# Performance work log

Measured on AMD Instinct MI355X. Metric: run time of the kernel, lower is better.

## Reference

```python
import jax, jax.numpy as jnp
import numpy as np

N, D, H, E = 50000, 512, 8, 3200000
DK = D // H  # 64


def setup_inputs() -> dict:
    key = jax.random.key(0)
    ks = jax.random.split(key, 12)
    x = jax.random.normal(ks[0], (N, D), dtype=jnp.float32)
    row_index = jnp.sort(jax.random.randint(ks[1], (E,), 0, N))
    col_index = jax.random.randint(ks[2], (E,), 0, N)
    att_bias = jax.random.normal(ks[3], (H, E), dtype=jnp.float32)
    # xavier-uniform-ish linear params (bias zero per module init)
    lim = np.sqrt(6.0 / (D + D)).astype(np.float32)
    def w(k):
        return jax.random.uniform(k, (D, D), minval=-lim, maxval=lim, dtype=jnp.float32)
    return {
        "x": x, "row_index": row_index, "col_index": col_index, "att_bias": att_bias,
        "Wq": w(ks[4]), "bq": jnp.zeros((D,), jnp.float32),
        "Wk": w(ks[5]), "bk": jnp.zeros((D,), jnp.float32),
        "Wv": w(ks[6]), "bv": jnp.zeros((D,), jnp.float32),
        "Wo": w(ks[7]), "bo": jnp.zeros((D,), jnp.float32),
    }


def _proj(x, W, b):
    # nn.Linear then reshape(N, H, DK).permute(1,0,2) -> [H, N, DK]
    return (x @ W.T + b).reshape(x.shape[0], H, DK).transpose(1, 0, 2)


def reference(x, row_index, col_index, att_bias, Wq, bq, Wk, bk, Wv, bv, Wo, bo):
    q = _proj(x, Wq, bq) / jnp.sqrt(jnp.float32(DK))  # [H,N,DK]
    k = _proj(x, Wk, bk)
    v = _proj(x, Wv, bv)
    n = x.shape[0]
    # masked QK^T at sparse (row,col) entries + additive sparse bias -> [H,E]
    logits = jnp.einsum("hed,hed->he", q[:, row_index], k[:, col_index]) + att_bias
    # per-row (segment) softmax over CSR rows, vmapped over heads
    seg_max = jax.vmap(lambda l: jax.ops.segment_max(l, row_index, num_segments=n))(logits)  # [H,N]
    p = jnp.exp(logits - seg_max[:, row_index])
    denom = jax.vmap(lambda pe: jax.ops.segment_sum(pe, row_index, num_segments=n))(p)  # [H,N]
    att = p / denom[:, row_index]  # [H,E]
    # sparse att @ V : scatter-add weighted value rows
    y = jax.vmap(lambda a, vc: jax.ops.segment_sum(a[:, None] * vc, row_index, num_segments=n))(
        att, v[:, col_index]
    )  # [H,N,DK]
    y = y.transpose(1, 0, 2).reshape(n, H * DK)  # [N,D]
    return y @ Wo.T + bo
```

## Files before the change

kernel.cpp:

```cpp
#include <hip/hip_runtime.h>
#include <hip/hip_bf16.h>
#include <cstddef>
#include <cstdint>


typedef __attribute__((ext_vector_type(8))) short bf16x8;
typedef __attribute__((ext_vector_type(4))) float f32x4;

#define KQ_SCALE 25.4f
#define KQ_DEQ   0.03937007874f

__device__ __forceinline__ void gload_lds16(const void* g, const void* l) {
    __builtin_amdgcn_global_load_lds(
        (const __attribute__((address_space(1))) unsigned int*)g,
        (__attribute__((address_space(3))) unsigned int*)l, 16, 0, 0);
}

__device__ __forceinline__ float bflo(unsigned u) { return __uint_as_float(u << 16); }
__device__ __forceinline__ float bfhi(unsigned u) { return __uint_as_float(u & 0xffff0000u); }
__device__ __forceinline__ float ub(unsigned u, int i) {
    return (float)((u >> (i * 8)) & 0xffu);
}

__device__ __forceinline__ void storeT(float* p, size_t i, float v) { p[i] = v; }
__device__ __forceinline__ void storeT(__hip_bfloat16* p, size_t i, float v) {
    p[i] = __float2bfloat16(v);
}
__device__ __forceinline__ void storeT(unsigned char* p, size_t i, float v) {
    const float q = fmaf(v, KQ_SCALE, 128.0f);
    p[i] = (unsigned char)__float2uint_rn(fminf(fmaxf(q, 0.f), 255.f));
}

__global__ __launch_bounds__(256) void conv_f32_bf16(
    const float* __restrict__ s, __hip_bfloat16* __restrict__ d, int n) {
    const int i = (blockIdx.x * 256 + threadIdx.x) * 8;
    if (i >= n) return;
    const float4 a = *(const float4*)(s + i);
    const float4 b = *(const float4*)(s + i + 4);
    alignas(16) __hip_bfloat16 o[8] = {
        __float2bfloat16(a.x), __float2bfloat16(a.y),
        __float2bfloat16(a.z), __float2bfloat16(a.w),
        __float2bfloat16(b.x), __float2bfloat16(b.y),
        __float2bfloat16(b.z), __float2bfloat16(b.w)};
    *(uint4*)(d + i) = *(const uint4*)o;
}

__global__ void row_start_kernel(const int* __restrict__ row_index,
                                 int* __restrict__ row_start, int n_rows, int E) {
    const int n = blockIdx.x * blockDim.x + threadIdx.x;
    if (n > n_rows) return;
    int lo = 0, hi = E;
    while (lo < hi) {
        const int mid = (lo + hi) >> 1;
        if (row_index[mid] < n) lo = mid + 1; else hi = mid;
    }
    row_start[n] = lo;
}

template <typename TO>
__global__ __launch_bounds__(256) void gemm_mfma_kernel(
    const short* __restrict__ A, const short* __restrict__ Bw,
    const float* __restrict__ bias, TO* __restrict__ C, int M, float scale) {
    __shared__ short As[128 * 32];
    __shared__ short Bs[128 * 32];
    const int t = threadIdx.x;
    const int w = t >> 6, l = t & 63;
    const int m0 = blockIdx.x * 128, n0 = blockIdx.y * 128;
    const int wrow = (w >> 1) * 64, wcol = (w & 1) * 64;
    const int fr = l & 15, fq = l >> 4;

    const int r0 = (w * 64 + l) >> 2, ko0 = ((w * 64 + l) & 3) * 8;
    int gmA0 = m0 + r0;      if (gmA0 >= M) gmA0 = M - 1;
    int gmA1 = m0 + r0 + 64; if (gmA1 >= M) gmA1 = M - 1;
    const int gnB0 = n0 + r0, gnB1 = n0 + r0 + 64;

    f32x4 acc[4][4];
#pragma unroll
    for (int mi = 0; mi < 4; ++mi)
#pragma unroll
        for (int ni = 0; ni < 4; ++ni) acc[mi][ni] = (f32x4){0.f, 0.f, 0.f, 0.f};

    for (int k0 = 0; k0 < 512; k0 += 32) {
        __syncthreads();
        gload_lds16(A + (size_t)gmA0 * 512 + k0 + ko0, As + w * 512);
        gload_lds16(A + (size_t)gmA1 * 512 + k0 + ko0, As + 2048 + w * 512);
        gload_lds16(Bw + (size_t)gnB0 * 512 + k0 + ko0, Bs + w * 512);
        gload_lds16(Bw + (size_t)gnB1 * 512 + k0 + ko0, Bs + 2048 + w * 512);
        __syncthreads();

        bf16x8 af[4], bfr[4];
#pragma unroll
        for (int mi = 0; mi < 4; ++mi)
            af[mi] = *(const bf16x8*)(As + (wrow + mi * 16 + fr) * 32 + fq * 8);
#pragma unroll
        for (int ni = 0; ni < 4; ++ni)
            bfr[ni] = *(const bf16x8*)(Bs + (wcol + ni * 16 + fr) * 32 + fq * 8);
#pragma unroll
        for (int mi = 0; mi < 4; ++mi)
#pragma unroll
            for (int ni = 0; ni < 4; ++ni)
                acc[mi][ni] = __builtin_amdgcn_mfma_f32_16x16x32_bf16(
                    af[mi], bfr[ni], acc[mi][ni], 0, 0, 0);
    }

#pragma unroll
    for (int mi = 0; mi < 4; ++mi)
#pragma unroll
        for (int ni = 0; ni < 4; ++ni)
#pragma unroll
            for (int r = 0; r < 4; ++r) {
                const int gr = m0 + wrow + mi * 16 + fq * 4 + r;
                if (gr < M) {
                    const int gc = n0 + wcol + ni * 16 + fr;
                    storeT(C, (size_t)gr * 512 + gc, (acc[mi][ni][r] + bias[gc]) * scale);
                }
            }
}

__global__ __launch_bounds__(256) void sparse_attn_kernel(
    const __hip_bfloat16* __restrict__ qb, const unsigned char* __restrict__ kq,
    const unsigned char* __restrict__ vq, const int* __restrict__ col_index,
    const float* __restrict__ att_bias, const int* __restrict__ row_start,
    __hip_bfloat16* __restrict__ yout, int E) {
    const int n = blockIdx.x;
    const int w = threadIdx.x >> 6;
    const int h = blockIdx.y * 4 + w;
    const int lane = threadIdx.x & 63;
    const int g = lane & 7;
    const int j = lane >> 3;
    const int e0 = row_start[n], e1 = row_start[n + 1];

    const size_t qrow = (size_t)n * 512 + h * 64;

    const uint4 qw = *(const uint4*)((const short*)qb + qrow + g * 8);
    float qf[8];
    {
        const unsigned* u = (const unsigned*)&qw;
#pragma unroll
        for (int i = 0; i < 4; ++i) { qf[2*i] = bflo(u[i]); qf[2*i+1] = bfhi(u[i]); }
    }
    float sumq = 0.f;
#pragma unroll
    for (int i = 0; i < 8; ++i) sumq += qf[i];
    const float qc = -128.0f * KQ_DEQ * sumq;

    const float* biasH = att_bias + (size_t)h * (size_t)E;
    const unsigned char* kh = kq + h * 64 + g * 8;
    const unsigned char* vh = vq + h * 64 + g * 8;

    float acc[8];
#pragma unroll
    for (int i = 0; i < 8; ++i) acc[i] = 0.f;
    float s = 0.f;

    if (e0 < e1) {
        const int e1m1 = e1 - 1;
        for (int base = e0; base < e1; base += 32) {
            int ec[4]; uint2 ku[4], vu[4]; float bv[4]; bool vld[4];
#pragma unroll
            for (int t = 0; t < 4; ++t) {
                const int e = base + t * 8 + j;
                vld[t] = e < e1;
                ec[t] = min(e, e1m1);
                const int c = col_index[ec[t]];
                ku[t] = *(const uint2*)(kh + (size_t)c * 512);
                vu[t] = *(const uint2*)(vh + (size_t)c * 512);
                bv[t] = biasH[ec[t]];
            }
            float d[4];
#pragma unroll
            for (int t = 0; t < 4; ++t) {
                float r0 = 0.f, r1 = 0.f;
#pragma unroll
                for (int i = 0; i < 4; ++i) {
                    r0 = fmaf(qf[i],     ub(ku[t].x, i), r0);
                    r1 = fmaf(qf[4 + i], ub(ku[t].y, i), r1);
                }
                d[t] = fmaf(KQ_DEQ, r0 + r1, qc);
            }
#pragma unroll
            for (int st = 1; st < 8; st <<= 1) {
#pragma unroll
                for (int t = 0; t < 4; ++t) d[t] += __shfl_xor(d[t], st, 64);
            }
            float p[4];
#pragma unroll
            for (int t = 0; t < 4; ++t)
                p[t] = vld[t] ? __expf(d[t] + bv[t]) : 0.f;

            float ps = (p[0] + p[1]) + (p[2] + p[3]);
#pragma unroll
            for (int st = 8; st < 64; st <<= 1) ps += __shfl_xor(ps, st, 64);
            s += ps;

#pragma unroll
            for (int t = 0; t < 4; ++t) {
#pragma unroll
                for (int i = 0; i < 4; ++i) {
                    acc[i]     = fmaf(p[t], ub(vu[t].x, i), acc[i]);
                    acc[4 + i] = fmaf(p[t], ub(vu[t].y, i), acc[4 + i]);
                }
            }
        }
    }

#pragma unroll
    for (int i = 0; i < 8; ++i) {
#pragma unroll
        for (int st = 8; st < 64; st <<= 1) acc[i] += __shfl_xor(acc[i], st, 64);
    }
    float yv = acc[0];
#pragma unroll
    for (int t = 1; t < 8; ++t) yv = (j == t) ? acc[t] : yv;
    const float r = (s > 0.f) ? fmaf(KQ_DEQ, yv / s, -128.0f * KQ_DEQ) : 0.f;
    yout[qrow + g * 8 + j] = __float2bfloat16(r);
}

extern "C" void kernel_launch(void* const* d_in, const int* in_sizes, int n_in,
                              void* d_out, int out_size, void* d_ws, size_t ws_size,
                              hipStream_t stream) {
    const float* x         = (const float*)d_in[0];
    const int*   row_index = (const int*)d_in[1];
    const int*   col_index = (const int*)d_in[2];
    const float* att_bias  = (const float*)d_in[3];
    const float* Wq = (const float*)d_in[4];
    const float* bq = (const float*)d_in[5];
    const float* Wk = (const float*)d_in[6];
    const float* bk = (const float*)d_in[7];
    const float* Wv = (const float*)d_in[8];
    const float* bv = (const float*)d_in[9];
    const float* Wo = (const float*)d_in[10];
    const float* bo = (const float*)d_in[11];
    float* out = (float*)d_out;

    const int N = in_sizes[0] / 512;
    const int E = in_sizes[1];
    const int WN = 512 * 512;

    char* ws = (char*)d_ws;
    const size_t nb = (size_t)N * 512 * sizeof(__hip_bfloat16);
    const size_t qb8 = (size_t)N * 512;
    const size_t wb = (size_t)WN * sizeof(__hip_bfloat16);
    __hip_bfloat16* xb  = (__hip_bfloat16*)(ws);
    __hip_bfloat16* qb  = (__hip_bfloat16*)(ws + nb);
    unsigned char*  kqv = (unsigned char*)(ws + 2 * nb);
    unsigned char*  vqv = (unsigned char*)(ws + 2 * nb + qb8);
    __hip_bfloat16* wqb = (__hip_bfloat16*)(ws + 2 * nb + 2 * qb8);
    __hip_bfloat16* wkb = (__hip_bfloat16*)(ws + 2 * nb + 2 * qb8 + wb);
    __hip_bfloat16* wvb = (__hip_bfloat16*)(ws + 2 * nb + 2 * qb8 + 2 * wb);
    __hip_bfloat16* wob = (__hip_bfloat16*)(ws + 2 * nb + 2 * qb8 + 3 * wb);
    int* row_start = (int*)(ws + 2 * nb + 2 * qb8 + 4 * wb);

    conv_f32_bf16<<<(N * 512 / 8 + 255) / 256, 256, 0, stream>>>(x, xb, N * 512);
    conv_f32_bf16<<<(WN / 8 + 255) / 256, 256, 0, stream>>>(Wq, wqb, WN);
    conv_f32_bf16<<<(WN / 8 + 255) / 256, 256, 0, stream>>>(Wk, wkb, WN);
    conv_f32_bf16<<<(WN / 8 + 255) / 256, 256, 0, stream>>>(Wv, wvb, WN);
    conv_f32_bf16<<<(WN / 8 + 255) / 256, 256, 0, stream>>>(Wo, wob, WN);

    row_start_kernel<<<(N + 1 + 255) / 256, 256, 0, stream>>>(row_index, row_start, N, E);

    const dim3 gg((N + 127) / 128, 4), gb(256);
    gemm_mfma_kernel<__hip_bfloat16><<<gg, gb, 0, stream>>>(
        (const short*)xb, (const short*)wqb, bq, qb, N, 0.125f);
    gemm_mfma_kernel<unsigned char><<<gg, gb, 0, stream>>>(
        (const short*)xb, (const short*)wkb, bk, kqv, N, 1.0f);
    gemm_mfma_kernel<unsigned char><<<gg, gb, 0, stream>>>(
        (const short*)xb, (const short*)wvb, bv, vqv, N, 1.0f);

    sparse_attn_kernel<<<dim3(N, 2), 256, 0, stream>>>(
        qb, kqv, vqv, col_index, att_bias, row_start, xb , E);

    gemm_mfma_kernel<float><<<gg, gb, 0, stream>>>(
        (const short*)xb, (const short*)wob, bo, out, N, 1.0f);
}
```

Baseline: 857.7 us.

## Process all heads per row block with 16-byte gathers and 8-edge steps

The sparse attention kernel now covers all 8 heads in one block per row: each wave handles two heads, and each lane covers 16 dims of one head. K and V rows are gathered with 16-byte loads instead of 8-byte loads, so each col_index read serves every head. The edge loop drops from 32-edge chunks with 4-way unrolling to 8-edge steps, and the row sum is reduced once after the loop rather than every iteration. The grid is halved to N blocks, which removes the duplicated col_index reads and per-row setup. This costs more registers per lane and leaves less memory-level parallelism per iteration.

```diff
diff --git a/kernel.cpp b/kernel.cpp
--- a/kernel.cpp
+++ b/kernel.cpp
@@ -124,96 +124,104 @@
     __hip_bfloat16* __restrict__ yout, int E) {
     const int n = blockIdx.x;
     const int w = threadIdx.x >> 6;
-    const int h = blockIdx.y * 4 + w;
     const int lane = threadIdx.x & 63;
     const int g = lane & 7;
     const int j = lane >> 3;
+    const int hA = 2 * w + (g >> 2);
+    const int dim0 = (g & 3) * 16;
     const int e0 = row_start[n], e1 = row_start[n + 1];
 
-    const size_t qrow = (size_t)n * 512 + h * 64;
-
-    const uint4 qw = *(const uint4*)((const short*)qb + qrow + g * 8);
-    float qf[8];
+    const short* qp = (const short*)qb + (size_t)n * 512 + hA * 64 + dim0;
+    float qf[16];
     {
-        const unsigned* u = (const unsigned*)&qw;
-#pragma unroll
-        for (int i = 0; i < 4; ++i) { qf[2*i] = bflo(u[i]); qf[2*i+1] = bfhi(u[i]); }
+        const uint4 a = *(const uint4*)qp;
+        const uint4 b = *(const uint4*)(qp + 8);
+        const unsigned* ua = (const unsigned*)&a;
+        const unsigned* ubp = (const unsigned*)&b;
+#pragma unroll
+        for (int i = 0; i < 4; ++i) {
+            qf[2 * i]     = bflo(ua[i]);
+            qf[2 * i + 1] = bfhi(ua[i]);
+            qf[8 + 2 * i]     = bflo(ubp[i]);
+            qf[8 + 2 * i + 1] = bfhi(ubp[i]);
+        }
     }
     float sumq = 0.f;
 #pragma unroll
-    for (int i = 0; i < 8; ++i) sumq += qf[i];
+    for (int i = 0; i < 16; ++i) sumq += qf[i];
+    sumq += __shfl_xor(sumq, 1, 64);
+    sumq += __shfl_xor(sumq, 2, 64);
     const float qc = -128.0f * KQ_DEQ * sumq;
 
-    const float* biasH = att_bias + (size_t)h * (size_t)E;
-    const unsigned char* kh = kq + h * 64 + g * 8;
-    const unsigned char* vh = vq + h * 64 + g * 8;
-
-    float acc[8];
-#pragma unroll
-    for (int i = 0; i < 8; ++i) acc[i] = 0.f;
-    float s = 0.f;
+    const float* biasH = att_bias + (size_t)hA * (size_t)E;
+    const unsigned pairoff = (unsigned)(w * 128 + g * 16);
+
+    float acc[16];
+#pragma unroll
+    for (int i = 0; i < 16; ++i) acc[i] = 0.f;
+    float s_lane = 0.f;
 
     if (e0 < e1) {
         const int e1m1 = e1 - 1;
-        for (int base = e0; base < e1; base += 32) {
-            int ec[4]; uint2 ku[4], vu[4]; float bv[4]; bool vld[4];
-#pragma unroll
-            for (int t = 0; t < 4; ++t) {
-                const int e = base + t * 8 + j;
-                vld[t] = e < e1;
-                ec[t] = min(e, e1m1);
-                const int c = col_index[ec[t]];
-                ku[t] = *(const uint2*)(kh + (size_t)c * 512);
-                vu[t] = *(const uint2*)(vh + (size_t)c * 512);
-                bv[t] = biasH[ec[t]];
+#pragma unroll 2
+        for (int base = e0; base < e1; base += 8) {
+            const int e = base + j;
+            const int ec = min(e, e1m1);
+            const int c = col_index[ec];
+            const unsigned co = ((unsigned)c << 9) + pairoff;
+            const uint4 ku = *(const uint4*)(kq + co);
+            const uint4 vu = *(const uint4*)(vq + co);
+            const float bv = biasH[ec];
+
+            float d = 0.f;
+            {
+                const unsigned* u = (const unsigned*)&ku;
+#pragma unroll
+                for (int i = 0; i < 4; ++i)
+#pragma unroll
+                    for (int b = 0; b < 4; ++b)
+                        d = fmaf(qf[4 * i + b], ub(u[i], b), d);
             }
-            float d[4];
-#pragma unroll
-            for (int t = 0; t < 4; ++t) {
-                float r0 = 0.f, r1 = 0.f;
-#pragma unroll
-                for (int i = 0; i < 4; ++i) {
-                    r0 = fmaf(qf[i],     ub(ku[t].x, i), r0);
-                    r1 = fmaf(qf[4 + i], ub(ku[t].y, i), r1);
-                }
-                d[t] = fmaf(KQ_DEQ, r0 + r1, qc);
-            }
-#pragma unroll
-            for (int st = 1; st < 8; st <<= 1) {
-#pragma unroll
-                for (int t = 0; t < 4; ++t) d[t] += __shfl_xor(d[t], st, 64);
-            }
-            float p[4];
-#pragma unroll
-            for (int t = 0; t < 4; ++t)
-                p[t] = vld[t] ? __expf(d[t] + bv[t]) : 0.f;
-
-            float ps = (p[0] + p[1]) + (p[2] + p[3]);
-#pragma unroll
-            for (int st = 8; st < 64; st <<= 1) ps += __shfl_xor(ps, st, 64);
-            s += ps;
-
-#pragma unroll
-            for (int t = 0; t < 4; ++t) {
-#pragma unroll
-                for (int i = 0; i < 4; ++i) {
-                    acc[i]     = fmaf(p[t], ub(vu[t].x, i), acc[i]);
-                    acc[4 + i] = fmaf(p[t], ub(vu[t].y, i), acc[4 + i]);
-                }
+            d += __shfl_xor(d, 1, 64);
+            d += __shfl_xor(d, 2, 64);
+            const float lg = fmaf(KQ_DEQ, d, qc) + bv;
+            const float p = (e < e1) ? __expf(lg) : 0.f;
+            s_lane += p;
+
+            {
+                const unsigned* u = (const unsigned*)&vu;
+#pragma unroll
+                for (int i = 0; i < 4; ++i)
+#pragma unroll
+                    for (int b = 0; b < 4; ++b)
+                        acc[4 * i + b] = fmaf(p, ub(u[i], b), acc[4 * i + b]);
             }
         }
     }
 
 #pragma unroll
-    for (int i = 0; i < 8; ++i) {
+    for (int st = 8; st < 64; st <<= 1) s_lane += __shfl_xor(s_lane, st, 64);
+#pragma unroll
+    for (int i = 0; i < 16; ++i) {
 #pragma unroll
         for (int st = 8; st < 64; st <<= 1) acc[i] += __shfl_xor(acc[i], st, 64);
     }
-    float yv = acc[0];
-#pragma unroll
-    for (int t = 1; t < 8; ++t) yv = (j == t) ? acc[t] : yv;
-    const float r = (s > 0.f) ? fmaf(KQ_DEQ, yv / s, -128.0f * KQ_DEQ) : 0.f;
-    yout[qrow + g * 8 + j] = __float2bfloat16(r);
+
+    float y0 = acc[0], y1 = acc[1];
+#pragma unroll
+    for (int t = 1; t < 8; ++t) {
+        y0 = (j == t) ? acc[2 * t] : y0;
+        y1 = (j == t) ? acc[2 * t + 1] : y1;
+    }
+    const size_t orow = (size_t)n * 512 + hA * 64 + dim0 + 2 * j;
+    if (s_lane > 0.f) {
+        const float inv = 1.0f / s_lane;
+        yout[orow]     = __float2bfloat16(fmaf(KQ_DEQ, y0 * inv, -128.0f * KQ_DEQ));
+        yout[orow + 1] = __float2bfloat16(fmaf(KQ_DEQ, y1 * inv, -128.0f * KQ_DEQ));
+    } else {
+        yout[orow]     = __float2bfloat16(0.f);
+        yout[orow + 1] = __float2bfloat16(0.f);
+    }
 }
 
 extern "C" void kernel_launch(void* const* d_in, const int* in_sizes, int n_in,
@@ -267,7 +275,7 @@
     gemm_mfma_kernel<unsigned char><<<gg, gb, 0, stream>>>(
         (const short*)xb, (const short*)wvb, bv, vqv, N, 1.0f);
 
-    sparse_attn_kernel<<<dim3(N, 2), 256, 0, stream>>>(
+    sparse_attn_kernel<<<N, 256, 0, stream>>>(
         qb, kqv, vqv, col_index, att_bias, row_start, xb , E);
 
     gemm_mfma_kernel<float><<<gg, gb, 0, stream>>>(
```

Result: faster. 778.9 us (-9.2%).
